# Kernel optimization log

Hardware: AMD Instinct MI355X
Metric: run time of the kernel (lower is better)

## Reference

```python
import jax, jax.numpy as jnp
import numpy as np

B, S, D, H, HD = 4096, 50, 32, 4, 8
SCALE = 1.0 / (8 ** 0.5)


def setup_inputs() -> dict:
    key = jax.random.key(0)
    ks = jax.random.split(key, 12)
    inp = {
        'Q': jax.random.normal(ks[0], (B, S, D), dtype=jnp.float32),
        'K': jax.random.normal(ks[1], (B, S, D), dtype=jnp.float32),
        'V': jax.random.normal(ks[2], (B, S, D), dtype=jnp.float32),
        'mask': jax.random.randint(ks[3], (B, 1, S, S), 0, 2).astype(jnp.bool_),
        # Linear weights (stored as [in, out]; equivalent math to torch's x @ W.T + b)
        'WQ': jax.random.normal(ks[4], (D, D), dtype=jnp.float32) * 0.1,
        'bQ': jnp.zeros((D,), dtype=jnp.float32),
        'WK': jax.random.normal(ks[5], (D, D), dtype=jnp.float32) * 0.1,
        'bK': jnp.zeros((D,), dtype=jnp.float32),
        'WV': jax.random.normal(ks[6], (D, D), dtype=jnp.float32) * 0.1,
        'bV': jnp.zeros((D,), dtype=jnp.float32),
        'WO': jax.random.normal(ks[7], (D, D), dtype=jnp.float32) * 0.1,
        'bO': jnp.zeros((D,), dtype=jnp.float32),
    }
    return inp


def reference(Q, K, V, mask, WQ, bQ, WK, bK, WV, bV, WO, bO):
    qSrc = Q
    # fcQ/fcK/fcV are (faithfully) applied twice, as in the original forward
    q = (Q @ WQ + bQ) @ WQ + bQ
    k = (K @ WK + bK) @ WK + bK
    v = (V @ WV + bV) @ WV + bV
    # split heads: [B, S, D] -> [B, H, S, HD]
    q = q.reshape(B, S, H, HD).transpose(0, 2, 1, 3)
    k = k.reshape(B, S, H, HD).transpose(0, 2, 1, 3)
    v = v.reshape(B, S, H, HD).transpose(0, 2, 1, 3)
    score = jnp.einsum('bhqd,bhkd->bhqk', q, k) * SCALE
    score = jnp.where(mask, -jnp.inf, score)
    attn = jax.nn.softmax(score, axis=-1)
    ctx = jnp.einsum('bhqk,bhkd->bhqd', attn, v)
    ctx = ctx.transpose(0, 2, 1, 3).reshape(B, S, D)
    out = ctx @ WO + bO  # dropout is identity in eval mode
    return qSrc + out
```

## Files before the change

kernel.cpp:

```cpp
#include <hip/hip_runtime.h>

#define NB 4096
constexpr float kQscale = 0.35355339059327378f * 1.4426950408889634f;

constexpr int ST = 40;
constexpr int SV = 72;
constexpr int OFF_W  = 0;
constexpr int OFF_V2 = 0;
constexpr int OFF_K2 = 5120;
constexpr int SH_LEN = 7680;

typedef __attribute__((ext_vector_type(8))) short bf16x8;
typedef __attribute__((ext_vector_type(4))) float f32x4;
typedef __attribute__((ext_vector_type(4))) unsigned u32x4;

__device__ __forceinline__ unsigned cvt2(float lo, float hi) {
  unsigned u;
  asm("v_cvt_pk_bf16_f32 %0, %1, %2" : "=v"(u) : "v"(lo), "v"(hi));
  return u;
}
__device__ __forceinline__ float fexp2(float x) {
  float r;
  asm("v_exp_f32 %0, %1" : "=v"(r) : "v"(x));
  return r;
}
__device__ __forceinline__ void xchF(unsigned& a, unsigned& b) {
  asm volatile("v_permlane32_swap_b32 %0, %1" : "+v"(a), "+v"(b));
  asm volatile("v_permlane16_swap_b32 %0, %1" : "+v"(a), "+v"(b));
}

__global__ __launch_bounds__(256) void mha(
    const float* __restrict__ Qg, const float* __restrict__ Kg,
    const float* __restrict__ Vg, const void* __restrict__ maskg,
    const float* __restrict__ WQg, const float* __restrict__ bQg,
    const float* __restrict__ WKg, const float* __restrict__ bKg,
    const float* __restrict__ WVg, const float* __restrict__ bVg,
    const float* __restrict__ WOg, const float* __restrict__ bOg,
    float* __restrict__ outg)
{
  __shared__ __align__(16) short SH[SH_LEN];
  __shared__ __align__(16) float sBias[128];
  __shared__ unsigned sRaw[80];

  const int t = threadIdx.x;
  const int b = blockIdx.x;
  const int lane = t & 63;
  const int wv = t >> 6;
  const int c = lane & 15, g = lane >> 4;
  const int myrow = wv*16 + c;

  auto mkfrag = [&](float4 x0, float4 x1) -> bf16x8 {
    const u32x4 u = {cvt2(x0.x,x0.y), cvt2(x0.z,x0.w), cvt2(x1.x,x1.y), cvt2(x1.z,x1.w)};
    return __builtin_bit_cast(bf16x8, u);
  };

  bf16x8 xbK, xbQ, xbV;
  {
    const int ra = b*1600 + ((myrow < 50) ? myrow : 0)*32 + g*8;
    const float4 ka = *(const float4*)&Kg[ra];
    const float4 kb = *(const float4*)&Kg[ra + 4];
    const float4 qa = *(const float4*)&Qg[ra];
    const float4 qc = *(const float4*)&Qg[ra + 4];
    const float4 va = *(const float4*)&Vg[ra];
    const float4 vb = *(const float4*)&Vg[ra + 4];
    xbK = mkfrag(ka, kb); xbQ = mkfrag(qa, qc); xbV = mkfrag(va, vb);
  }

  const unsigned w64det = ((const unsigned*)maskg)[lane];
  unsigned valB[10];
  #pragma unroll
  for (int cc = 0; cc < 10; ++cc) {
    const int idx = (wv*10 + cc)*64 + lane;
    valB[cc] = (idx < 2500) ? (unsigned)((const unsigned char*)maskg)[b*2500 + idx] : 0u;
  }
  {
    const int wd = t & 31, wk0 = (t >> 5) * 4;
    #pragma unroll
    for (int m = 0; m < 4; ++m) {
      const float* Wp = (m == 0) ? WQg : (m == 1) ? WKg : (m == 2) ? WVg : WOg;
      const float w0 = Wp[(wk0+0)*32 + wd];
      const float w1 = Wp[(wk0+1)*32 + wd];
      const float w2 = Wp[(wk0+2)*32 + wd];
      const float w3 = Wp[(wk0+3)*32 + wd];
      *(uint2*)&SH[OFF_W + m*1280 + wd*ST + wk0] = make_uint2(cvt2(w0,w1), cvt2(w2,w3));
    }
  }
  if      (t < 32)  sBias[t] = bQg[t];
  else if (t < 64)  sBias[t] = bKg[t-32];
  else if (t < 96)  sBias[t] = bVg[t-64];
  else if (t < 128) sBias[t] = bOg[t-96];
  {
    const bool byteMask = (__ballot(w64det > 1u) != 0ull);
    #pragma unroll
    for (int cc = 0; cc < 10; ++cc) {
      const int ch = wv*10 + cc;
      const int idx = ch*64 + lane;
      unsigned val;
      if (byteMask) val = valB[cc];
      else          val = (idx < 2500) ? ((const unsigned*)maskg)[b*2500 + idx] : 0u;
      const unsigned long long m = __ballot(val != 0u);
      if (lane == 0) {
        sRaw[ch*2]     = (unsigned)m;
        sRaw[ch*2 + 1] = (unsigned)(m >> 32);
      }
    }
  }
  __syncthreads();

  unsigned mm0, mm1;
  {
    const int bp = (myrow < 50) ? 50*myrow : 0;
    const unsigned ra = sRaw[(bp >> 5) + 0];
    const unsigned rb = sRaw[(bp >> 5) + 1];
    const unsigned rc = sRaw[(bp >> 5) + 2];
    const unsigned sh = bp & 31;
    mm0 = (unsigned)((((unsigned long long)rb << 32) | ra) >> sh);
    mm1 = (unsigned)((((unsigned long long)rc << 32) | rb) >> sh);
    if (myrow >= 50) { mm0 = ~0u; mm1 = ~0u; }
  }

  auto projR = [&](bf16x8 xb, int wm, int biasOff, float scale) -> bf16x8 {
    const bf16x8 wa0 = *(const bf16x8*)&SH[OFF_W + wm*1280 + c*ST + g*8];
    const bf16x8 wa1 = *(const bf16x8*)&SH[OFF_W + wm*1280 + (16 + c)*ST + g*8];
    const float4 bv0 = *(const float4*)&sBias[biasOff + g*4];
    const float4 bv1 = *(const float4*)&sBias[biasOff + 16 + g*4];
    f32x4 c0 = {bv0.x, bv0.y, bv0.z, bv0.w};
    f32x4 c1 = {bv1.x, bv1.y, bv1.z, bv1.w};
    c0 = __builtin_amdgcn_mfma_f32_16x16x32_bf16(wa0, xb, c0, 0, 0, 0);
    c1 = __builtin_amdgcn_mfma_f32_16x16x32_bf16(wa1, xb, c1, 0, 0, 0);
    unsigned A0 = cvt2(c0[0]*scale, c0[1]*scale), A1 = cvt2(c0[2]*scale, c0[3]*scale);
    unsigned B0 = cvt2(c1[0]*scale, c1[1]*scale), B1 = cvt2(c1[2]*scale, c1[3]*scale);
    xchF(A0, B0); xchF(A1, B1);
    const u32x4 u = {A0, A1, B0, B1};
    return __builtin_bit_cast(bf16x8, u);
  };

  const bf16x8 k1f = projR(xbK, 1, 32, 1.f);
  const bf16x8 v1f = projR(xbV, 2, 64, 1.f);
  const bf16x8 q1f = projR(xbQ, 0, 0,  1.f);
  {
    #pragma unroll
    for (int Ni = 0; Ni < 2; ++Ni) {
      const bf16x8 wa = *(const bf16x8*)&SH[OFF_W + 1*1280 + (Ni*16 + c)*ST + g*8];
      const float4 bv = *(const float4*)&sBias[32 + Ni*16 + g*4];
      f32x4 acc = {bv.x, bv.y, bv.z, bv.w};
      acc = __builtin_amdgcn_mfma_f32_16x16x32_bf16(wa, k1f, acc, 0, 0, 0);
      *(uint2*)&SH[OFF_K2 + myrow*ST + Ni*16 + g*4] =
          make_uint2(cvt2(acc[0], acc[1]), cvt2(acc[2], acc[3]));
    }
  }
  const bf16x8 qb = projR(q1f, 0, 0, kQscale);
  f32x4 vacc0, vacc1;
  {
    const bf16x8 wb0 = *(const bf16x8*)&SH[OFF_W + 2*1280 + c*ST + g*8];
    const bf16x8 wb1 = *(const bf16x8*)&SH[OFF_W + 2*1280 + (16 + c)*ST + g*8];
    const float bv0 = sBias[64 + c], bv1 = sBias[64 + 16 + c];
    f32x4 z0 = {bv0, bv0, bv0, bv0}, z1 = {bv1, bv1, bv1, bv1};
    vacc0 = __builtin_amdgcn_mfma_f32_16x16x32_bf16(v1f, wb0, z0, 0, 0, 0);
    vacc1 = __builtin_amdgcn_mfma_f32_16x16x32_bf16(v1f, wb1, z1, 0, 0, 0);
  }
  __syncthreads();

  {
    const int j0 = wv*16 + g*4;
    const float v0 = (j0+0 < 50) ? vacc0[0] : 0.f;
    const float v1 = (j0+1 < 50) ? vacc0[1] : 0.f;
    const float v2 = (j0+2 < 50) ? vacc0[2] : 0.f;
    const float v3 = (j0+3 < 50) ? vacc0[3] : 0.f;
    *(uint2*)&SH[OFF_V2 + c*SV + j0] = make_uint2(cvt2(v0,v1), cvt2(v2,v3));
    const float u0 = (j0+0 < 50) ? vacc1[0] : 0.f;
    const float u1 = (j0+1 < 50) ? vacc1[1] : 0.f;
    const float u2 = (j0+2 < 50) ? vacc1[2] : 0.f;
    const float u3 = (j0+3 < 50) ? vacc1[3] : 0.f;
    *(uint2*)&SH[OFF_V2 + (16 + c)*SV + j0] = make_uint2(cvt2(u0,u1), cvt2(u2,u3));
  }
  bf16x8 kf[4];
  #pragma unroll
  for (int Ni = 0; Ni < 4; ++Ni)
    kf[Ni] = *(const bf16x8*)&SH[OFF_K2 + (Ni*16 + c)*ST + g*8];
  __syncthreads();

  const bf16x8 zf = {0,0,0,0,0,0,0,0};
  unsigned ox0[4], ox1[4];
  #pragma unroll
  for (int h = 0; h < 4; ++h) {
    const bf16x8 vf0 = *(const bf16x8*)&SH[OFF_V2 + (h*8 + (c & 7))*SV + g*8];
    const bf16x8 vf1 = *(const bf16x8*)&SH[OFF_V2 + (h*8 + (c & 7))*SV + 32 + g*8];
    const bf16x8 qh = (g == h) ? qb : zf;
    unsigned pk[8];
    float rs = 0.f;
    #pragma unroll
    for (int Ni = 0; Ni < 4; ++Ni) {
      f32x4 z = {0.f, 0.f, 0.f, 0.f};
      const f32x4 s = __builtin_amdgcn_mfma_f32_16x16x32_bf16(kf[Ni], qh, z, 0, 0, 0);
      const unsigned w = (Ni < 2) ? mm0 : mm1;
      float p[4];
      #pragma unroll
      for (int r = 0; r < 4; ++r) {
        const int key = Ni*16 + g*4 + r;
        const bool keep = (key < 50) && (((w >> (key & 31)) & 1u) == 0u);
        p[r] = keep ? fexp2(s[r]) : 0.f;
        rs += p[r];
      }
      pk[Ni*2]   = cvt2(p[0], p[1]);
      pk[Ni*2+1] = cvt2(p[2], p[3]);
    }
    rs += __shfl_xor(rs, 16);
    rs += __shfl_xor(rs, 32);
    const float ri = __builtin_amdgcn_rcpf(rs);
    unsigned w0 = pk[0], w2 = pk[2];  xchF(w0, w2);
    unsigned w1 = pk[1], w3 = pk[3];  xchF(w1, w3);
    unsigned x0 = pk[4], x2 = pk[6];  xchF(x0, x2);
    unsigned x1 = pk[5], x3 = pk[7];  xchF(x1, x3);
    const u32x4 w0v = {w0, w1, w2, w3};
    const u32x4 w1v = {x0, x1, x2, x3};
    const bf16x8 pf0 = __builtin_bit_cast(bf16x8, w0v);
    const bf16x8 pf1 = __builtin_bit_cast(bf16x8, w1v);
    f32x4 cac = {0.f, 0.f, 0.f, 0.f};
    cac = __builtin_amdgcn_mfma_f32_16x16x32_bf16(vf0, pf0, cac, 0, 0, 0);
    cac = __builtin_amdgcn_mfma_f32_16x16x32_bf16(vf1, pf1, cac, 0, 0, 0);
    ox0[h] = cvt2(cac[0]*ri, cac[1]*ri);
    ox1[h] = cvt2(cac[2]*ri, cac[3]*ri);
  }

  {
    float res[2][4];
    #pragma unroll
    for (int Nj = 0; Nj < 2; ++Nj)
      #pragma unroll
      for (int r = 0; r < 4; ++r) {
        const int row = wv*16 + g*4 + r;
        res[Nj][r] = (row < 50) ? Qg[b*1600 + row*32 + Nj*16 + c] : 0.f;
      }
    unsigned a0 = ox0[0], a1 = ox0[1], a2 = ox0[2], a3 = ox0[3];
    xchF(a0, a1);
    xchF(a2, a3);
    xchF(a0, a2);
    xchF(a1, a3);
    unsigned c0 = ox1[0], c1 = ox1[1], c2 = ox1[2], c3 = ox1[3];
    xchF(c0, c1);
    xchF(c2, c3);
    xchF(c0, c2);
    xchF(c1, c3);
    const u32x4 afv = {a0, c0, a1, c1};
    const bf16x8 af = __builtin_bit_cast(bf16x8, afv);
    #pragma unroll
    for (int Nj = 0; Nj < 2; ++Nj) {
      const bf16x8 bbf = *(const bf16x8*)&SH[OFF_W + 3*1280 + (Nj*16 + c)*ST + g*8];
      const float bv = sBias[96 + Nj*16 + c];
      f32x4 o = {bv, bv, bv, bv};
      o = __builtin_amdgcn_mfma_f32_16x16x32_bf16(af, bbf, o, 0, 0, 0);
      #pragma unroll
      for (int r = 0; r < 4; ++r) {
        const int row = wv*16 + g*4 + r;
        if (row < 50)
          outg[b*1600 + row*32 + Nj*16 + c] = o[r] + res[Nj][r];
      }
    }
  }
}

extern "C" void kernel_launch(void* const* d_in, const int* in_sizes, int n_in,
                              void* d_out, int out_size, void* d_ws, size_t ws_size,
                              hipStream_t stream) {
  const float* Q  = (const float*)d_in[0];
  const float* K  = (const float*)d_in[1];
  const float* V  = (const float*)d_in[2];
  const void*  M  = d_in[3];
  const float* WQ = (const float*)d_in[4];
  const float* bQ = (const float*)d_in[5];
  const float* WK = (const float*)d_in[6];
  const float* bK = (const float*)d_in[7];
  const float* WV = (const float*)d_in[8];
  const float* bV = (const float*)d_in[9];
  const float* WO = (const float*)d_in[10];
  const float* bO = (const float*)d_in[11];
  float* out = (float*)d_out;
  (void)d_ws; (void)ws_size; (void)in_sizes; (void)n_in; (void)out_size;

  hipLaunchKernelGGL(mha, dim3(NB), dim3(256), 0, stream,
                     Q, K, V, M, WQ, bQ, WK, bK, WV, bV, WO, bO, out);
}
```

Measured before the change: 54.62 us.

## Map one batch element per wavefront and loop over query tiles

Result: slower. 65.07 us (+19.1%).

```diff
diff --git a/kernel.cpp b/kernel.cpp
--- a/kernel.cpp
+++ b/kernel.cpp
@@ -2,13 +2,7 @@
 
 #define NB 4096
 constexpr float kQscale = 0.35355339059327378f * 1.4426950408889634f;
-
-constexpr int ST = 40;
 constexpr int SV = 72;
-constexpr int OFF_W  = 0;
-constexpr int OFF_V2 = 0;
-constexpr int OFF_K2 = 5120;
-constexpr int SH_LEN = 7680;
 
 typedef __attribute__((ext_vector_type(8))) short bf16x8;
 typedef __attribute__((ext_vector_type(4))) float f32x4;
@@ -38,92 +32,30 @@
     const float* __restrict__ WOg, const float* __restrict__ bOg,
     float* __restrict__ outg)
 {
-  __shared__ __align__(16) short SH[SH_LEN];
-  __shared__ __align__(16) float sBias[128];
-  __shared__ unsigned sRaw[80];
+  __shared__ __align__(16) short V2s[4][32*SV];
+  __shared__ unsigned sRawW[4][80];
 
   const int t = threadIdx.x;
-  const int b = blockIdx.x;
   const int lane = t & 63;
   const int wv = t >> 6;
   const int c = lane & 15, g = lane >> 4;
-  const int myrow = wv*16 + c;
+  const int b = blockIdx.x*4 + wv;
+  short* V2 = V2s[wv];
+  unsigned* sRaw = sRawW[wv];
 
   auto mkfrag = [&](float4 x0, float4 x1) -> bf16x8 {
     const u32x4 u = {cvt2(x0.x,x0.y), cvt2(x0.z,x0.w), cvt2(x1.x,x1.y), cvt2(x1.z,x1.w)};
     return __builtin_bit_cast(bf16x8, u);
   };
-
-  bf16x8 xbK, xbQ, xbV;
-  {
-    const int ra = b*1600 + ((myrow < 50) ? myrow : 0)*32 + g*8;
-    const float4 ka = *(const float4*)&Kg[ra];
-    const float4 kb = *(const float4*)&Kg[ra + 4];
-    const float4 qa = *(const float4*)&Qg[ra];
-    const float4 qc = *(const float4*)&Qg[ra + 4];
-    const float4 va = *(const float4*)&Vg[ra];
-    const float4 vb = *(const float4*)&Vg[ra + 4];
-    xbK = mkfrag(ka, kb); xbQ = mkfrag(qa, qc); xbV = mkfrag(va, vb);
-  }
-
-  const unsigned w64det = ((const unsigned*)maskg)[lane];
-  unsigned valB[10];
-  #pragma unroll
-  for (int cc = 0; cc < 10; ++cc) {
-    const int idx = (wv*10 + cc)*64 + lane;
-    valB[cc] = (idx < 2500) ? (unsigned)((const unsigned char*)maskg)[b*2500 + idx] : 0u;
-  }
-  {
-    const int wd = t & 31, wk0 = (t >> 5) * 4;
-    #pragma unroll
-    for (int m = 0; m < 4; ++m) {
-      const float* Wp = (m == 0) ? WQg : (m == 1) ? WKg : (m == 2) ? WVg : WOg;
-      const float w0 = Wp[(wk0+0)*32 + wd];
-      const float w1 = Wp[(wk0+1)*32 + wd];
-      const float w2 = Wp[(wk0+2)*32 + wd];
-      const float w3 = Wp[(wk0+3)*32 + wd];
-      *(uint2*)&SH[OFF_W + m*1280 + wd*ST + wk0] = make_uint2(cvt2(w0,w1), cvt2(w2,w3));
-    }
-  }
-  if      (t < 32)  sBias[t] = bQg[t];
-  else if (t < 64)  sBias[t] = bKg[t-32];
-  else if (t < 96)  sBias[t] = bVg[t-64];
-  else if (t < 128) sBias[t] = bOg[t-96];
-  {
-    const bool byteMask = (__ballot(w64det > 1u) != 0ull);
-    #pragma unroll
-    for (int cc = 0; cc < 10; ++cc) {
-      const int ch = wv*10 + cc;
-      const int idx = ch*64 + lane;
-      unsigned val;
-      if (byteMask) val = valB[cc];
-      else          val = (idx < 2500) ? ((const unsigned*)maskg)[b*2500 + idx] : 0u;
-      const unsigned long long m = __ballot(val != 0u);
-      if (lane == 0) {
-        sRaw[ch*2]     = (unsigned)m;
-        sRaw[ch*2 + 1] = (unsigned)(m >> 32);
-      }
-    }
-  }
-  __syncthreads();
-
-  unsigned mm0, mm1;
-  {
-    const int bp = (myrow < 50) ? 50*myrow : 0;
-    const unsigned ra = sRaw[(bp >> 5) + 0];
-    const unsigned rb = sRaw[(bp >> 5) + 1];
-    const unsigned rc = sRaw[(bp >> 5) + 2];
-    const unsigned sh = bp & 31;
-    mm0 = (unsigned)((((unsigned long long)rb << 32) | ra) >> sh);
-    mm1 = (unsigned)((((unsigned long long)rc << 32) | rb) >> sh);
-    if (myrow >= 50) { mm0 = ~0u; mm1 = ~0u; }
-  }
-
-  auto projR = [&](bf16x8 xb, int wm, int biasOff, float scale) -> bf16x8 {
-    const bf16x8 wa0 = *(const bf16x8*)&SH[OFF_W + wm*1280 + c*ST + g*8];
-    const bf16x8 wa1 = *(const bf16x8*)&SH[OFF_W + wm*1280 + (16 + c)*ST + g*8];
-    const float4 bv0 = *(const float4*)&sBias[biasOff + g*4];
-    const float4 bv1 = *(const float4*)&sBias[biasOff + 16 + g*4];
+  auto ldW = [&](const float* __restrict__ Wp, int dcol) -> bf16x8 {
+    float w[8];
+    #pragma unroll
+    for (int e = 0; e < 8; ++e) w[e] = Wp[(g*8 + e)*32 + dcol];
+    const u32x4 u = {cvt2(w[0],w[1]), cvt2(w[2],w[3]), cvt2(w[4],w[5]), cvt2(w[6],w[7])};
+    return __builtin_bit_cast(bf16x8, u);
+  };
+  auto projR = [&](bf16x8 xb, bf16x8 wa0, bf16x8 wa1,
+                   float4 bv0, float4 bv1, float scale) -> bf16x8 {
     f32x4 c0 = {bv0.x, bv0.y, bv0.z, bv0.w};
     f32x4 c1 = {bv1.x, bv1.y, bv1.z, bv1.w};
     c0 = __builtin_amdgcn_mfma_f32_16x16x32_bf16(wa0, xb, c0, 0, 0, 0);
@@ -135,126 +67,192 @@
     return __builtin_bit_cast(bf16x8, u);
   };
 
-  const bf16x8 k1f = projR(xbK, 1, 32, 1.f);
-  const bf16x8 v1f = projR(xbV, 2, 64, 1.f);
-  const bf16x8 q1f = projR(xbQ, 0, 0,  1.f);
   {
-    #pragma unroll
-    for (int Ni = 0; Ni < 2; ++Ni) {
-      const bf16x8 wa = *(const bf16x8*)&SH[OFF_W + 1*1280 + (Ni*16 + c)*ST + g*8];
-      const float4 bv = *(const float4*)&sBias[32 + Ni*16 + g*4];
-      f32x4 acc = {bv.x, bv.y, bv.z, bv.w};
-      acc = __builtin_amdgcn_mfma_f32_16x16x32_bf16(wa, k1f, acc, 0, 0, 0);
-      *(uint2*)&SH[OFF_K2 + myrow*ST + Ni*16 + g*4] =
-          make_uint2(cvt2(acc[0], acc[1]), cvt2(acc[2], acc[3]));
-    }
-  }
-  const bf16x8 qb = projR(q1f, 0, 0, kQscale);
-  f32x4 vacc0, vacc1;
+    const unsigned wdet = ((const unsigned*)maskg)[lane];
+    const bool byteMask = (__ballot(wdet > 1u) != 0ull);
+    for (int cg = 0; cg < 5; ++cg) {
+      unsigned v[8];
+      #pragma unroll
+      for (int j = 0; j < 8; ++j) {
+        const int idx = (cg*8 + j)*64 + lane;
+        v[j] = 0;
+        if (idx < 2500)
+          v[j] = byteMask ? (unsigned)((const unsigned char*)maskg)[b*2500 + idx]
+                          : ((const unsigned*)maskg)[b*2500 + idx];
+      }
+      #pragma unroll
+      for (int j = 0; j < 8; ++j) {
+        const unsigned long long m = __ballot(v[j] != 0u);
+        const int ch = cg*8 + j;
+        if (lane < 2) sRaw[ch*2 + lane] = lane ? (unsigned)(m >> 32) : (unsigned)m;
+      }
+    }
+  }
+
+  bf16x8 kf[4];
   {
-    const bf16x8 wb0 = *(const bf16x8*)&SH[OFF_W + 2*1280 + c*ST + g*8];
-    const bf16x8 wb1 = *(const bf16x8*)&SH[OFF_W + 2*1280 + (16 + c)*ST + g*8];
-    const float bv0 = sBias[64 + c], bv1 = sBias[64 + 16 + c];
-    f32x4 z0 = {bv0, bv0, bv0, bv0}, z1 = {bv1, bv1, bv1, bv1};
-    vacc0 = __builtin_amdgcn_mfma_f32_16x16x32_bf16(v1f, wb0, z0, 0, 0, 0);
-    vacc1 = __builtin_amdgcn_mfma_f32_16x16x32_bf16(v1f, wb1, z1, 0, 0, 0);
-  }
+    const bf16x8 wK0 = ldW(WKg, c), wK1 = ldW(WKg, 16 + c);
+    const float4 bK0 = *(const float4*)&bKg[g*4];
+    const float4 bK1 = *(const float4*)&bKg[16 + g*4];
+    #pragma unroll
+    for (int m = 0; m < 4; ++m) {
+      const int row = m*16 + c;
+      const int ra = b*1600 + ((row < 50) ? row : 0)*32 + g*8;
+      const bf16x8 xb = mkfrag(*(const float4*)&Kg[ra], *(const float4*)&Kg[ra + 4]);
+      const bf16x8 k1 = projR(xb, wK0, wK1, bK0, bK1, 1.f);
+      kf[m] = projR(k1, wK0, wK1, bK0, bK1, 1.f);
+    }
+  }
+
+  {
+    const bf16x8 wV0 = ldW(WVg, c), wV1 = ldW(WVg, 16 + c);
+    const float4 bV0 = *(const float4*)&bVg[g*4];
+    const float4 bV1 = *(const float4*)&bVg[16 + g*4];
+    const float bc0 = bVg[c], bc1 = bVg[16 + c];
+    #pragma unroll
+    for (int m = 0; m < 4; ++m) {
+      const int row = m*16 + c;
+      const int ra = b*1600 + ((row < 50) ? row : 0)*32 + g*8;
+      const bf16x8 xb = mkfrag(*(const float4*)&Vg[ra], *(const float4*)&Vg[ra + 4]);
+      const bf16x8 v1 = projR(xb, wV0, wV1, bV0, bV1, 1.f);
+      f32x4 z0 = {bc0, bc0, bc0, bc0}, z1 = {bc1, bc1, bc1, bc1};
+      z0 = __builtin_amdgcn_mfma_f32_16x16x32_bf16(v1, wV0, z0, 0, 0, 0);
+      z1 = __builtin_amdgcn_mfma_f32_16x16x32_bf16(v1, wV1, z1, 0, 0, 0);
+      const int j0 = m*16 + g*4;
+      const float a0 = (j0+0 < 50) ? z0[0] : 0.f;
+      const float a1 = (j0+1 < 50) ? z0[1] : 0.f;
+      const float a2 = (j0+2 < 50) ? z0[2] : 0.f;
+      const float a3 = (j0+3 < 50) ? z0[3] : 0.f;
+      *(uint2*)&V2[c*SV + j0] = make_uint2(cvt2(a0,a1), cvt2(a2,a3));
+      const float u0 = (j0+0 < 50) ? z1[0] : 0.f;
+      const float u1 = (j0+1 < 50) ? z1[1] : 0.f;
+      const float u2 = (j0+2 < 50) ? z1[2] : 0.f;
+      const float u3 = (j0+3 < 50) ? z1[3] : 0.f;
+      *(uint2*)&V2[(16 + c)*SV + j0] = make_uint2(cvt2(u0,u1), cvt2(u2,u3));
+    }
+  }
+
+  const bf16x8 wQ0 = ldW(WQg, c), wQ1 = ldW(WQg, 16 + c);
+  const float4 bQ0 = *(const float4*)&bQg[g*4];
+  const float4 bQ1 = *(const float4*)&bQg[16 + g*4];
+  const bf16x8 wO0 = ldW(WOg, c), wO1 = ldW(WOg, 16 + c);
+  const float bO0 = bOg[c], bO1 = bOg[16 + c];
   __syncthreads();
 
-  {
-    const int j0 = wv*16 + g*4;
-    const float v0 = (j0+0 < 50) ? vacc0[0] : 0.f;
-    const float v1 = (j0+1 < 50) ? vacc0[1] : 0.f;
-    const float v2 = (j0+2 < 50) ? vacc0[2] : 0.f;
-    const float v3 = (j0+3 < 50) ? vacc0[3] : 0.f;
-    *(uint2*)&SH[OFF_V2 + c*SV + j0] = make_uint2(cvt2(v0,v1), cvt2(v2,v3));
-    const float u0 = (j0+0 < 50) ? vacc1[0] : 0.f;
-    const float u1 = (j0+1 < 50) ? vacc1[1] : 0.f;
-    const float u2 = (j0+2 < 50) ? vacc1[2] : 0.f;
-    const float u3 = (j0+3 < 50) ? vacc1[3] : 0.f;
-    *(uint2*)&SH[OFF_V2 + (16 + c)*SV + j0] = make_uint2(cvt2(u0,u1), cvt2(u2,u3));
-  }
-  bf16x8 kf[4];
-  #pragma unroll
-  for (int Ni = 0; Ni < 4; ++Ni)
-    kf[Ni] = *(const bf16x8*)&SH[OFF_K2 + (Ni*16 + c)*ST + g*8];
-  __syncthreads();
-
   const bf16x8 zf = {0,0,0,0,0,0,0,0};
-  unsigned ox0[4], ox1[4];
-  #pragma unroll
-  for (int h = 0; h < 4; ++h) {
-    const bf16x8 vf0 = *(const bf16x8*)&SH[OFF_V2 + (h*8 + (c & 7))*SV + g*8];
-    const bf16x8 vf1 = *(const bf16x8*)&SH[OFF_V2 + (h*8 + (c & 7))*SV + 32 + g*8];
-    const bf16x8 qh = (g == h) ? qb : zf;
-    unsigned pk[8];
-    float rs = 0.f;
-    #pragma unroll
-    for (int Ni = 0; Ni < 4; ++Ni) {
-      f32x4 z = {0.f, 0.f, 0.f, 0.f};
-      const f32x4 s = __builtin_amdgcn_mfma_f32_16x16x32_bf16(kf[Ni], qh, z, 0, 0, 0);
-      const unsigned w = (Ni < 2) ? mm0 : mm1;
-      float p[4];
-      #pragma unroll
-      for (int r = 0; r < 4; ++r) {
-        const int key = Ni*16 + g*4 + r;
-        const bool keep = (key < 50) && (((w >> (key & 31)) & 1u) == 0u);
-        p[r] = keep ? fexp2(s[r]) : 0.f;
-        rs += p[r];
-      }
-      pk[Ni*2]   = cvt2(p[0], p[1]);
-      pk[Ni*2+1] = cvt2(p[2], p[3]);
-    }
-    rs += __shfl_xor(rs, 16);
-    rs += __shfl_xor(rs, 32);
-    const float ri = __builtin_amdgcn_rcpf(rs);
-    unsigned w0 = pk[0], w2 = pk[2];  xchF(w0, w2);
-    unsigned w1 = pk[1], w3 = pk[3];  xchF(w1, w3);
-    unsigned x0 = pk[4], x2 = pk[6];  xchF(x0, x2);
-    unsigned x1 = pk[5], x3 = pk[7];  xchF(x1, x3);
-    const u32x4 w0v = {w0, w1, w2, w3};
-    const u32x4 w1v = {x0, x1, x2, x3};
-    const bf16x8 pf0 = __builtin_bit_cast(bf16x8, w0v);
-    const bf16x8 pf1 = __builtin_bit_cast(bf16x8, w1v);
-    f32x4 cac = {0.f, 0.f, 0.f, 0.f};
-    cac = __builtin_amdgcn_mfma_f32_16x16x32_bf16(vf0, pf0, cac, 0, 0, 0);
-    cac = __builtin_amdgcn_mfma_f32_16x16x32_bf16(vf1, pf1, cac, 0, 0, 0);
-    ox0[h] = cvt2(cac[0]*ri, cac[1]*ri);
-    ox1[h] = cvt2(cac[2]*ri, cac[3]*ri);
-  }
-
-  {
-    float res[2][4];
-    #pragma unroll
-    for (int Nj = 0; Nj < 2; ++Nj)
-      #pragma unroll
-      for (int r = 0; r < 4; ++r) {
-        const int row = wv*16 + g*4 + r;
-        res[Nj][r] = (row < 50) ? Qg[b*1600 + row*32 + Nj*16 + c] : 0.f;
-      }
-    unsigned a0 = ox0[0], a1 = ox0[1], a2 = ox0[2], a3 = ox0[3];
-    xchF(a0, a1);
-    xchF(a2, a3);
-    xchF(a0, a2);
-    xchF(a1, a3);
-    unsigned c0 = ox1[0], c1 = ox1[1], c2 = ox1[2], c3 = ox1[3];
-    xchF(c0, c1);
-    xchF(c2, c3);
-    xchF(c0, c2);
-    xchF(c1, c3);
-    const u32x4 afv = {a0, c0, a1, c1};
-    const bf16x8 af = __builtin_bit_cast(bf16x8, afv);
-    #pragma unroll
-    for (int Nj = 0; Nj < 2; ++Nj) {
-      const bf16x8 bbf = *(const bf16x8*)&SH[OFF_W + 3*1280 + (Nj*16 + c)*ST + g*8];
-      const float bv = sBias[96 + Nj*16 + c];
-      f32x4 o = {bv, bv, bv, bv};
-      o = __builtin_amdgcn_mfma_f32_16x16x32_bf16(af, bbf, o, 0, 0, 0);
-      #pragma unroll
-      for (int r = 0; r < 4; ++r) {
-        const int row = wv*16 + g*4 + r;
-        if (row < 50)
-          outg[b*1600 + row*32 + Nj*16 + c] = o[r] + res[Nj][r];
+
+  #pragma unroll 1
+  for (int qt = 0; qt < 4; ++qt) {
+    const int myq = qt*16 + c;
+    bf16x8 qb;
+    {
+      const int ra = b*1600 + ((myq < 50) ? myq : 0)*32 + g*8;
+      const bf16x8 xq = mkfrag(*(const float4*)&Qg[ra], *(const float4*)&Qg[ra + 4]);
+      const bf16x8 q1 = projR(xq, wQ0, wQ1, bQ0, bQ1, 1.f);
+      qb = projR(q1, wQ0, wQ1, bQ0, bQ1, kQscale);
+    }
+    unsigned mm0, mm1;
+    {
+      const int bp = (myq < 50) ? 50*myq : 0;
+      const unsigned ra = sRaw[(bp >> 5) + 0];
+      const unsigned rb = sRaw[(bp >> 5) + 1];
+      const unsigned rc = sRaw[(bp >> 5) + 2];
+      const unsigned sh = bp & 31;
+      mm0 = (unsigned)((((unsigned long long)rb << 32) | ra) >> sh);
+      mm1 = (unsigned)((((unsigned long long)rc << 32) | rb) >> sh);
+      if (myq >= 50) { mm0 = ~0u; mm1 = ~0u; }
+    }
+    unsigned ox0[4], ox1[4];
+    #pragma unroll
+    for (int h = 0; h < 4; ++h) {
+      const bf16x8 vf0 = *(const bf16x8*)&V2[(h*8 + (c & 7))*SV + g*8];
+      const bf16x8 vf1 = *(const bf16x8*)&V2[(h*8 + (c & 7))*SV + 32 + g*8];
+      const bf16x8 qh = (g == h) ? qb : zf;
+      f32x4 sc[4];
+      #pragma unroll
+      for (int Ni = 0; Ni < 4; ++Ni) {
+        f32x4 z = {0.f, 0.f, 0.f, 0.f};
+        sc[Ni] = __builtin_amdgcn_mfma_f32_16x16x32_bf16(kf[Ni], qh, z, 0, 0, 0);
+      }
+      unsigned kpm = 0;
+      float mx = -1e30f;
+      #pragma unroll
+      for (int Ni = 0; Ni < 4; ++Ni) {
+        const unsigned w = (Ni < 2) ? mm0 : mm1;
+        #pragma unroll
+        for (int r = 0; r < 4; ++r) {
+          const int key = Ni*16 + g*4 + r;
+          const bool keep = (key < 50) && (((w >> (key & 31)) & 1u) == 0u);
+          kpm |= keep ? (1u << (Ni*4 + r)) : 0u;
+          mx = keep ? fmaxf(mx, sc[Ni][r]) : mx;
+        }
+      }
+      mx = fmaxf(mx, __shfl_xor(mx, 16));
+      mx = fmaxf(mx, __shfl_xor(mx, 32));
+      float rs = 0.f;
+      unsigned pk[8];
+      #pragma unroll
+      for (int Ni = 0; Ni < 4; ++Ni) {
+        float p[4];
+        #pragma unroll
+        for (int r = 0; r < 4; ++r) {
+          const float e = fexp2(sc[Ni][r] - mx);
+          p[r] = ((kpm >> (Ni*4 + r)) & 1u) ? e : 0.f;
+          rs += p[r];
+        }
+        pk[Ni*2]   = cvt2(p[0], p[1]);
+        pk[Ni*2+1] = cvt2(p[2], p[3]);
+      }
+      rs += __shfl_xor(rs, 16);
+      rs += __shfl_xor(rs, 32);
+      const float ri = (rs > 0.f) ? __builtin_amdgcn_rcpf(rs) : 0.f;
+      unsigned w0 = pk[0], w2 = pk[2];  xchF(w0, w2);
+      unsigned w1 = pk[1], w3 = pk[3];  xchF(w1, w3);
+      unsigned x0 = pk[4], x2 = pk[6];  xchF(x0, x2);
+      unsigned x1 = pk[5], x3 = pk[7];  xchF(x1, x3);
+      const u32x4 w0v = {w0, w1, w2, w3};
+      const u32x4 w1v = {x0, x1, x2, x3};
+      const bf16x8 pf0 = __builtin_bit_cast(bf16x8, w0v);
+      const bf16x8 pf1 = __builtin_bit_cast(bf16x8, w1v);
+      f32x4 cac = {0.f, 0.f, 0.f, 0.f};
+      cac = __builtin_amdgcn_mfma_f32_16x16x32_bf16(vf0, pf0, cac, 0, 0, 0);
+      cac = __builtin_amdgcn_mfma_f32_16x16x32_bf16(vf1, pf1, cac, 0, 0, 0);
+      ox0[h] = cvt2(cac[0]*ri, cac[1]*ri);
+      ox1[h] = cvt2(cac[2]*ri, cac[3]*ri);
+    }
+    {
+      float res[2][4];
+      #pragma unroll
+      for (int Nj = 0; Nj < 2; ++Nj)
+        #pragma unroll
+        for (int r = 0; r < 4; ++r) {
+          const int row = qt*16 + g*4 + r;
+          res[Nj][r] = (row < 50) ? Qg[b*1600 + row*32 + Nj*16 + c] : 0.f;
+        }
+      unsigned a0 = ox0[0], a1 = ox0[1], a2 = ox0[2], a3 = ox0[3];
+      xchF(a0, a1);
+      xchF(a2, a3);
+      xchF(a0, a2);
+      xchF(a1, a3);
+      unsigned c0 = ox1[0], c1 = ox1[1], c2 = ox1[2], c3 = ox1[3];
+      xchF(c0, c1);
+      xchF(c2, c3);
+      xchF(c0, c2);
+      xchF(c1, c3);
+      const u32x4 afv = {a0, c0, a1, c1};
+      const bf16x8 af = __builtin_bit_cast(bf16x8, afv);
+      #pragma unroll
+      for (int Nj = 0; Nj < 2; ++Nj) {
+        const bf16x8 bbf = Nj ? wO1 : wO0;
+        const float bv = Nj ? bO1 : bO0;
+        f32x4 o = {bv, bv, bv, bv};
+        o = __builtin_amdgcn_mfma_f32_16x16x32_bf16(af, bbf, o, 0, 0, 0);
+        #pragma unroll
+        for (int r = 0; r < 4; ++r) {
+          const int row = qt*16 + g*4 + r;
+          if (row < 50)
+            outg[b*1600 + row*32 + Nj*16 + c] = o[r] + res[Nj][r];
+        }
       }
     }
   }
@@ -278,6 +276,6 @@
   float* out = (float*)d_out;
   (void)d_ws; (void)ws_size; (void)in_sizes; (void)n_in; (void)out_size;
 
-  hipLaunchKernelGGL(mha, dim3(NB), dim3(256), 0, stream,
+  hipLaunchKernelGGL(mha, dim3(NB/4), dim3(256), 0, stream,
                      Q, K, V, M, WQ, bQ, WK, bK, WV, bV, WO, bO, out);
 }
```
